# Optimization experiments

Hardware: AMD Instinct MI355X
Metric: run time of the kernel (lower is better)

The kernel has to match this reference:

```python
import jax, jax.numpy as jnp
import numpy as np


def setup_inputs() -> dict:
    key = jax.random.key(0)
    k1, k2 = jax.random.split(key)
    set1 = jax.random.normal(k1, (8, 4096, 3), dtype=jnp.float32)
    set2 = jax.random.normal(k2, (8, 4096, 3), dtype=jnp.float32)
    return {"set1": set1, "set2": set2}


def reference(set1, set2):
    # set1: [b, n, d], set2: [b, m, d]
    n = set1.shape[1]
    x2 = jnp.sum(set1 * set1, axis=-1)            # [b, n]
    y2 = jnp.sum(set2 * set2, axis=-1)            # [b, m]
    xy = jnp.einsum('bnd,bmd->bnm', set1, set2)   # [b, n, m]
    d2 = x2[:, :, None] + y2[:, None, :] - 2.0 * xy
    dist = jnp.sqrt(jnp.maximum(d2, 0.0))         # torch.cdist(p=2)
    out_dist = jnp.min(dist, axis=2)              # [b, n]
    out_dist2 = jnp.min(dist, axis=1)             # [b, m]
    total = jnp.mean(out_dist) + jnp.mean(out_dist2)
    return total / n
```

## Files before the change

### kernel.cpp

```cpp
#include <hip/hip_runtime.h>
#include <math.h>
#include <float.h>


#define BATCH   8
#define NPTS    4096
#define THREADS 512
#define QB      128
#define QPT     4
#define NGRP    16
#define PPG     (NPTS/NGRP)

__global__ __launch_bounds__(THREADS, 4)
void chamfer_main(const float* __restrict__ set1,
                  const float* __restrict__ set2,
                  float* __restrict__ out)
{
    __shared__ float4 dbp[NPTS];
    __shared__ float  part[NGRP][QB];

    const int blk = blockIdx.x;
    const int dir = blk >> 8;
    const int rem = blk & 255;
    const int b   = rem >> 5;
    const int qb  = rem & 31;

    const float* __restrict__ Q  = dir ? set2 : set1;
    const float* __restrict__ DB = dir ? set1 : set2;
    const float* __restrict__ DBb = DB + (size_t)b * NPTS * 3;

    const int t = threadIdx.x;

    for (int i = t; i < NPTS; i += THREADS) {
        const float x = DBb[3 * i + 0];
        const float y = DBb[3 * i + 1];
        const float z = DBb[3 * i + 2];
        dbp[i] = make_float4(x, y, z, fmaf(x, x, fmaf(y, y, z * z)));
    }

    const int l = t & 31;
    const int g = t >> 5;
    const int qbase = qb * QB;

    float qa[QPT], qbc[QPT], qc[QPT], dmin[QPT];
    #pragma unroll
    for (int j = 0; j < QPT; ++j) {
        const float* qp = Q + ((size_t)b * NPTS + qbase + l + 32 * j) * 3;
        qa[j]  = -2.0f * qp[0];
        qbc[j] = -2.0f * qp[1];
        qc[j]  = -2.0f * qp[2];
        dmin[j] = FLT_MAX;
    }

    __syncthreads();

    const float4* __restrict__ s4 = dbp + g * PPG;

    #pragma unroll 2
    for (int c = 0; c < PPG / 4; ++c) {
        const float4 P0 = s4[c * 4 + 0];
        const float4 P1 = s4[c * 4 + 1];
        const float4 P2 = s4[c * 4 + 2];
        const float4 P3 = s4[c * 4 + 3];
        #pragma unroll
        for (int j = 0; j < QPT; ++j) {
            const float a = qa[j], bb = qbc[j], cc = qc[j];
            float d0 = fmaf(a, P0.x, fmaf(bb, P0.y, fmaf(cc, P0.z, P0.w)));
            float d1 = fmaf(a, P1.x, fmaf(bb, P1.y, fmaf(cc, P1.z, P1.w)));
            float d2 = fmaf(a, P2.x, fmaf(bb, P2.y, fmaf(cc, P2.z, P2.w)));
            float d3 = fmaf(a, P3.x, fmaf(bb, P3.y, fmaf(cc, P3.z, P3.w)));
            dmin[j] = fminf(dmin[j], fminf(fminf(d0, d1), fminf(d2, d3)));
        }
    }

    #pragma unroll
    for (int j = 0; j < QPT; ++j)
        part[g][l + 32 * j] = dmin[j];
    __syncthreads();

    float dist = 0.0f;
    if (t < QB) {
        float m = part[0][t];
        #pragma unroll
        for (int gg = 1; gg < NGRP; ++gg)
            m = fminf(m, part[gg][t]);
        const float* qp = Q + ((size_t)b * NPTS + qbase + t) * 3;
        const float qx = qp[0], qy = qp[1], qz = qp[2];
        const float q2 = fmaf(qx, qx, fmaf(qy, qy, qz * qz));
        dist = sqrtf(fmaxf(q2 + m, 0.0f));
    }

    #pragma unroll
    for (int off = 32; off > 0; off >>= 1)
        dist += __shfl_down(dist, off);
    if (t < QB && (t & 63) == 0)
        atomicAdd(out, dist * (1.0f / (float)((size_t)BATCH * NPTS * NPTS)));
}

extern "C" void kernel_launch(void* const* d_in, const int* in_sizes, int n_in,
                              void* d_out, int out_size, void* d_ws, size_t ws_size,
                              hipStream_t stream) {
    const float* s1 = (const float*)d_in[0];
    const float* s2 = (const float*)d_in[1];
    float* out = (float*)d_out;

    hipMemsetAsync(out, 0, sizeof(float), stream);
    chamfer_main<<<dim3(512), dim3(THREADS), 0, stream>>>(s1, s2, out);
}
```

Baseline: 82.86 us.

## Double block size and per-thread queries, vectorize DB staging, reduce partials via shuffles

Each block now has 1024 threads handling 256 queries, with 8 queries per thread, so only 256 blocks are launched. The database point cloud is staged into shared memory with three float4 loads per thread instead of strided scalar loads. Partial minima from the two 32-lane halves of each 64-wide wavefront are combined with a shuffle, which halves the shared partial array. The larger register footprint (8 queries per thread) and fewer blocks (256 on a large GPU) may reduce occupancy and leave compute units idle.

```diff
diff --git a/kernel.cpp b/kernel.cpp
--- a/kernel.cpp
+++ b/kernel.cpp
@@ -5,10 +5,10 @@
 
 #define BATCH   8
 #define NPTS    4096
-#define THREADS 512
-#define QB      128
-#define QPT     4
-#define NGRP    16
+#define THREADS 1024
+#define QB      256
+#define QPT     8
+#define NGRP    32
 #define PPG     (NPTS/NGRP)
 
 __global__ __launch_bounds__(THREADS, 4)
@@ -17,13 +17,13 @@
                   float* __restrict__ out)
 {
     __shared__ float4 dbp[NPTS];
-    __shared__ float  part[NGRP][QB];
+    __shared__ float  part[NGRP / 2][QB];
 
     const int blk = blockIdx.x;
-    const int dir = blk >> 8;
-    const int rem = blk & 255;
-    const int b   = rem >> 5;
-    const int qb  = rem & 31;
+    const int dir = blk >> 7;
+    const int rem = blk & 127;
+    const int b   = rem >> 4;
+    const int qb  = rem & 15;
 
     const float* __restrict__ Q  = dir ? set2 : set1;
     const float* __restrict__ DB = dir ? set1 : set2;
@@ -31,11 +31,19 @@
 
     const int t = threadIdx.x;
 
-    for (int i = t; i < NPTS; i += THREADS) {
-        const float x = DBb[3 * i + 0];
-        const float y = DBb[3 * i + 1];
-        const float z = DBb[3 * i + 2];
-        dbp[i] = make_float4(x, y, z, fmaf(x, x, fmaf(y, y, z * z)));
+    {
+        const float4* g4 = (const float4*)DBb;
+        const float4 r0 = g4[3 * t + 0];
+        const float4 r1 = g4[3 * t + 1];
+        const float4 r2 = g4[3 * t + 2];
+        dbp[4 * t + 0] = make_float4(r0.x, r0.y, r0.z,
+                                     fmaf(r0.x, r0.x, fmaf(r0.y, r0.y, r0.z * r0.z)));
+        dbp[4 * t + 1] = make_float4(r0.w, r1.x, r1.y,
+                                     fmaf(r0.w, r0.w, fmaf(r1.x, r1.x, r1.y * r1.y)));
+        dbp[4 * t + 2] = make_float4(r1.z, r1.w, r2.x,
+                                     fmaf(r1.z, r1.z, fmaf(r1.w, r1.w, r2.x * r2.x)));
+        dbp[4 * t + 3] = make_float4(r2.y, r2.z, r2.w,
+                                     fmaf(r2.y, r2.y, fmaf(r2.z, r2.z, r2.w * r2.w)));
     }
 
     const int l = t & 31;
@@ -69,32 +77,35 @@
             float d1 = fmaf(a, P1.x, fmaf(bb, P1.y, fmaf(cc, P1.z, P1.w)));
             float d2 = fmaf(a, P2.x, fmaf(bb, P2.y, fmaf(cc, P2.z, P2.w)));
             float d3 = fmaf(a, P3.x, fmaf(bb, P3.y, fmaf(cc, P3.z, P3.w)));
-            dmin[j] = fminf(dmin[j], fminf(fminf(d0, d1), fminf(d2, d3)));
+            dmin[j] = fminf(fminf(fminf(d0, d1), d2), fminf(fminf(d3, dmin[j]), dmin[j]));
         }
     }
 
+    const int w = t >> 6;
     #pragma unroll
-    for (int j = 0; j < QPT; ++j)
-        part[g][l + 32 * j] = dmin[j];
+    for (int j = 0; j < QPT; ++j) {
+        const float other = __shfl_down(dmin[j], 32);
+        if (l == (t & 63))
+            part[w][l + 32 * j] = fminf(dmin[j], other);
+    }
     __syncthreads();
 
-    float dist = 0.0f;
     if (t < QB) {
         float m = part[0][t];
         #pragma unroll
-        for (int gg = 1; gg < NGRP; ++gg)
-            m = fminf(m, part[gg][t]);
+        for (int ww = 1; ww < NGRP / 2; ++ww)
+            m = fminf(m, part[ww][t]);
         const float* qp = Q + ((size_t)b * NPTS + qbase + t) * 3;
         const float qx = qp[0], qy = qp[1], qz = qp[2];
         const float q2 = fmaf(qx, qx, fmaf(qy, qy, qz * qz));
-        dist = sqrtf(fmaxf(q2 + m, 0.0f));
+        float dist = sqrtf(fmaxf(q2 + m, 0.0f));
+
+        #pragma unroll
+        for (int off = 32; off > 0; off >>= 1)
+            dist += __shfl_down(dist, off);
+        if ((t & 63) == 0)
+            atomicAdd(out, dist * (1.0f / 134217728.0f));
     }
-
-    #pragma unroll
-    for (int off = 32; off > 0; off >>= 1)
-        dist += __shfl_down(dist, off);
-    if (t < QB && (t & 63) == 0)
-        atomicAdd(out, dist * (1.0f / (float)((size_t)BATCH * NPTS * NPTS)));
 }
 
 extern "C" void kernel_launch(void* const* d_in, const int* in_sizes, int n_in,
@@ -105,5 +116,5 @@
     float* out = (float*)d_out;
 
     hipMemsetAsync(out, 0, sizeof(float), stream);
-    chamfer_main<<<dim3(512), dim3(THREADS), 0, stream>>>(s1, s2, out);
+    chamfer_main<<<dim3(256), dim3(THREADS), 0, stream>>>(s1, s2, out);
 }
```

Measured after the change: 89.61 us. 1.08x slower.

## Prepack points into float4 workspace and read database directly from global memory

Applied to the files above, without the earlier changes.

Adds a pre-pass kernel that converts both point sets into float4 records with squared norms, plus a second copy holding the query coordinates scaled by -2. The main kernel drops its per-block shared-memory staging of the database and instead has each wavefront read its slice of points straight from global/L2 using wave-uniform addresses. Block size doubles to 1024 threads, each block covering 256 queries with 64-lane wavefronts. This removes the redundant per-block strided AoS loads and the LDS fill barrier, at the cost of an extra kernel launch, workspace traffic, and fewer, larger blocks (256 over the GPU's CUs).

```diff
diff --git a/kernel.cpp b/kernel.cpp
--- a/kernel.cpp
+++ b/kernel.cpp
@@ -5,96 +5,104 @@
 
 #define BATCH   8
 #define NPTS    4096
-#define THREADS 512
-#define QB      128
+#define NSET    (BATCH * NPTS)
+#define THREADS 1024
+#define QB      256
 #define QPT     4
-#define NGRP    16
-#define PPG     (NPTS/NGRP)
+#define NW      (THREADS / 64)
+#define PPW     (NPTS / NW)
+
+__global__ __launch_bounds__(256)
+void pack_points(const float* __restrict__ s1, const float* __restrict__ s2,
+                 float4* __restrict__ ws)
+{
+    const int t   = blockIdx.x * 256 + threadIdx.x;
+    const int set = t >> 13;
+    const int tp  = t & 8191;
+    const float* __restrict__ src = set ? s2 : s1;
+
+    const float4* g4 = (const float4*)src;
+    const float4 r0 = g4[3 * tp + 0];
+    const float4 r1 = g4[3 * tp + 1];
+    const float4 r2 = g4[3 * tp + 2];
+
+    float px[4] = {r0.x, r0.w, r1.z, r2.y};
+    float py[4] = {r0.y, r1.x, r1.w, r2.z};
+    float pz[4] = {r0.z, r1.y, r2.x, r2.w};
+
+    const int base = set * NSET + 4 * tp;
+    #pragma unroll
+    for (int k = 0; k < 4; ++k) {
+        const float n = fmaf(px[k], px[k], fmaf(py[k], py[k], pz[k] * pz[k]));
+        ws[base + k]            = make_float4(px[k], py[k], pz[k], n);
+        ws[2 * NSET + base + k] = make_float4(-2.0f * px[k], -2.0f * py[k],
+                                              -2.0f * pz[k], n);
+    }
+}
 
 __global__ __launch_bounds__(THREADS, 4)
-void chamfer_main(const float* __restrict__ set1,
-                  const float* __restrict__ set2,
-                  float* __restrict__ out)
+void chamfer_main(const float4* __restrict__ ws, float* __restrict__ out)
 {
-    __shared__ float4 dbp[NPTS];
-    __shared__ float  part[NGRP][QB];
+    __shared__ float part[NW][QB];
 
     const int blk = blockIdx.x;
-    const int dir = blk >> 8;
-    const int rem = blk & 255;
-    const int b   = rem >> 5;
-    const int qb  = rem & 31;
+    const int dir = blk >> 7;
+    const int b   = (blk >> 4) & 7;
+    const int qb  = blk & 15;
 
-    const float* __restrict__ Q  = dir ? set2 : set1;
-    const float* __restrict__ DB = dir ? set1 : set2;
-    const float* __restrict__ DBb = DB + (size_t)b * NPTS * 3;
+    const float4* __restrict__ P  = ws + ((dir ^ 1) * BATCH + b) * NPTS;
+    const float4* __restrict__ Qc = ws + 2 * NSET + (dir * BATCH + b) * NPTS + qb * QB;
 
     const int t = threadIdx.x;
+    const int l = t & 63;
+    const int w = __builtin_amdgcn_readfirstlane(t >> 6);
 
-    for (int i = t; i < NPTS; i += THREADS) {
-        const float x = DBb[3 * i + 0];
-        const float y = DBb[3 * i + 1];
-        const float z = DBb[3 * i + 2];
-        dbp[i] = make_float4(x, y, z, fmaf(x, x, fmaf(y, y, z * z)));
-    }
-
-    const int l = t & 31;
-    const int g = t >> 5;
-    const int qbase = qb * QB;
-
-    float qa[QPT], qbc[QPT], qc[QPT], dmin[QPT];
+    float qa[QPT], qbv[QPT], qcv[QPT], dmin[QPT];
     #pragma unroll
     for (int j = 0; j < QPT; ++j) {
-        const float* qp = Q + ((size_t)b * NPTS + qbase + l + 32 * j) * 3;
-        qa[j]  = -2.0f * qp[0];
-        qbc[j] = -2.0f * qp[1];
-        qc[j]  = -2.0f * qp[2];
+        const float4 q = Qc[j * 64 + l];
+        qa[j] = q.x; qbv[j] = q.y; qcv[j] = q.z;
         dmin[j] = FLT_MAX;
     }
 
-    __syncthreads();
-
-    const float4* __restrict__ s4 = dbp + g * PPG;
+    const float4* __restrict__ S = P + w * PPW;
 
     #pragma unroll 2
-    for (int c = 0; c < PPG / 4; ++c) {
-        const float4 P0 = s4[c * 4 + 0];
-        const float4 P1 = s4[c * 4 + 1];
-        const float4 P2 = s4[c * 4 + 2];
-        const float4 P3 = s4[c * 4 + 3];
+    for (int c = 0; c < PPW; c += 4) {
+        const float4 P0 = S[c + 0];
+        const float4 P1 = S[c + 1];
+        const float4 P2 = S[c + 2];
+        const float4 P3 = S[c + 3];
         #pragma unroll
         for (int j = 0; j < QPT; ++j) {
-            const float a = qa[j], bb = qbc[j], cc = qc[j];
-            float d0 = fmaf(a, P0.x, fmaf(bb, P0.y, fmaf(cc, P0.z, P0.w)));
-            float d1 = fmaf(a, P1.x, fmaf(bb, P1.y, fmaf(cc, P1.z, P1.w)));
-            float d2 = fmaf(a, P2.x, fmaf(bb, P2.y, fmaf(cc, P2.z, P2.w)));
-            float d3 = fmaf(a, P3.x, fmaf(bb, P3.y, fmaf(cc, P3.z, P3.w)));
+            const float a = qa[j], bb = qbv[j], cc = qcv[j];
+            const float d0 = fmaf(a, P0.x, fmaf(bb, P0.y, fmaf(cc, P0.z, P0.w)));
+            const float d1 = fmaf(a, P1.x, fmaf(bb, P1.y, fmaf(cc, P1.z, P1.w)));
+            const float d2 = fmaf(a, P2.x, fmaf(bb, P2.y, fmaf(cc, P2.z, P2.w)));
+            const float d3 = fmaf(a, P3.x, fmaf(bb, P3.y, fmaf(cc, P3.z, P3.w)));
             dmin[j] = fminf(dmin[j], fminf(fminf(d0, d1), fminf(d2, d3)));
         }
     }
 
     #pragma unroll
     for (int j = 0; j < QPT; ++j)
-        part[g][l + 32 * j] = dmin[j];
+        part[w][j * 64 + l] = dmin[j];
     __syncthreads();
 
-    float dist = 0.0f;
     if (t < QB) {
         float m = part[0][t];
         #pragma unroll
-        for (int gg = 1; gg < NGRP; ++gg)
-            m = fminf(m, part[gg][t]);
-        const float* qp = Q + ((size_t)b * NPTS + qbase + t) * 3;
-        const float qx = qp[0], qy = qp[1], qz = qp[2];
-        const float q2 = fmaf(qx, qx, fmaf(qy, qy, qz * qz));
-        dist = sqrtf(fmaxf(q2 + m, 0.0f));
+        for (int ww = 1; ww < NW; ++ww)
+            m = fminf(m, part[ww][t]);
+        const float qw = Qc[t].w;
+        float dist = sqrtf(fmaxf(qw + m, 0.0f));
+
+        #pragma unroll
+        for (int off = 32; off > 0; off >>= 1)
+            dist += __shfl_down(dist, off);
+        if ((t & 63) == 0)
+            atomicAdd(out, dist * (1.0f / 134217728.0f));
     }
-
-    #pragma unroll
-    for (int off = 32; off > 0; off >>= 1)
-        dist += __shfl_down(dist, off);
-    if (t < QB && (t & 63) == 0)
-        atomicAdd(out, dist * (1.0f / (float)((size_t)BATCH * NPTS * NPTS)));
 }
 
 extern "C" void kernel_launch(void* const* d_in, const int* in_sizes, int n_in,
@@ -103,7 +111,9 @@
     const float* s1 = (const float*)d_in[0];
     const float* s2 = (const float*)d_in[1];
     float* out = (float*)d_out;
+    float4* ws = (float4*)d_ws;
 
     hipMemsetAsync(out, 0, sizeof(float), stream);
-    chamfer_main<<<dim3(512), dim3(THREADS), 0, stream>>>(s1, s2, out);
+    pack_points<<<dim3(64), dim3(256), 0, stream>>>(s1, s2, ws);
+    chamfer_main<<<dim3(256), dim3(THREADS), 0, stream>>>(ws, out);
 }
```

Measured after the change: 101.7 us. 22.8% more time.
